# Optimization experiments

Hardware: AMD Instinct MI355X
Metric: run time of the kernel (lower is better)

## Reference

```python
import jax, jax.numpy as jnp
import numpy as np

B, L, E, H, RR, BIO, NT, V, R = 16, 128, 256, 256, 128, 64, 3, 30000, 25


def setup_inputs() -> dict:
    key = jax.random.key(0)
    ks = jax.random.split(key, 24)
    s = 0.05
    n = jax.random.normal
    inp = {
        'tokens': jax.random.randint(ks[0], (B, L), 0, V),
        'bio_gold': jax.random.randint(ks[1], (B, L), 0, NT),
        'selection_gold': jax.random.uniform(ks[2], (B, L, R, L), jnp.float32),
        'word_emb': n(ks[3], (V, E), jnp.float32) * s,
        'W_ih_f': n(ks[4], (4 * H, E), jnp.float32) * s,
        'W_hh_f': n(ks[5], (4 * H, H), jnp.float32) * s,
        'b_f': n(ks[6], (4 * H,), jnp.float32) * s,
        'W_ih_b': n(ks[7], (4 * H, E), jnp.float32) * s,
        'W_hh_b': n(ks[8], (4 * H, H), jnp.float32) * s,
        'b_b': n(ks[9], (4 * H,), jnp.float32) * s,
        'emi_W': n(ks[10], (NT, H), jnp.float32) * s,
        'emi_b': n(ks[11], (NT,), jnp.float32) * s,
        'bio_emb': n(ks[12], (NT + 1, BIO), jnp.float32) * s,
        'sel_u_W': n(ks[13], (RR, H + BIO), jnp.float32) * s,
        'sel_u_b': n(ks[14], (RR,), jnp.float32) * s,
        'sel_v_W': n(ks[15], (RR, H + BIO), jnp.float32) * s,
        'sel_v_b': n(ks[16], (RR,), jnp.float32) * s,
        'sel_uv_W': n(ks[17], (RR, 2 * RR), jnp.float32) * s,
        'sel_uv_b': n(ks[18], (RR,), jnp.float32) * s,
        'rel_emb': n(ks[19], (R, RR), jnp.float32) * s,
        'crf_start': n(ks[20], (NT,), jnp.float32) * s,
        'crf_end': n(ks[21], (NT,), jnp.float32) * s,
        'crf_trans': n(ks[22], (NT, NT), jnp.float32) * s,
    }
    return inp


def _lstm(x, W_ih, W_hh, b, reverse):
    # x: [B,L,E] -> hidden states [B,L,H]; PyTorch gate order i,f,g,o
    Bb = x.shape[0]
    Hh = W_hh.shape[1]
    xg = jnp.swapaxes(jnp.einsum('ble,ge->blg', x, W_ih) + b, 0, 1)  # [L,B,4H]

    def step(carry, xt):
        h, c = carry
        g = xt + h @ W_hh.T
        i, f, gg, o = jnp.split(g, 4, axis=-1)
        c = jax.nn.sigmoid(f) * c + jax.nn.sigmoid(i) * jnp.tanh(gg)
        h = jax.nn.sigmoid(o) * jnp.tanh(c)
        return (h, c), h

    init = (jnp.zeros((Bb, Hh), x.dtype), jnp.zeros((Bb, Hh), x.dtype))
    _, hs = jax.lax.scan(step, init, xg, reverse=reverse)
    return jnp.swapaxes(hs, 0, 1)


def reference(tokens, bio_gold, selection_gold, word_emb, W_ih_f, W_hh_f, b_f,
              W_ih_b, W_hh_b, b_b, emi_W, emi_b, bio_emb, sel_u_W, sel_u_b,
              sel_v_W, sel_v_b, sel_uv_W, sel_uv_b, rel_emb, crf_start,
              crf_end, crf_trans):
    mask = tokens != 0  # pad id 0
    maskf = mask.astype(jnp.float32)
    emb = word_emb[tokens]
    # BiLSTM, halves averaged as in (fwd + bwd) / 2
    o = (_lstm(emb, W_ih_f, W_hh_f, b_f, False)
         + _lstm(emb, W_ih_b, W_hh_b, b_b, True)) * 0.5
    emi = o @ emi_W.T + emi_b  # [B,L,NT]

    # ---- CRF negative log-likelihood (torchcrf, reduction='mean') ----
    bidx = jnp.arange(tokens.shape[0])
    e_sel = jnp.take_along_axis(emi, bio_gold[..., None], axis=2)[..., 0]  # [B,L]
    num = crf_start[bio_gold[:, 0]] + e_sel[:, 0]
    tr = crf_trans[bio_gold[:, :-1], bio_gold[:, 1:]]  # [B,L-1]
    num = num + ((tr + e_sel[:, 1:]) * maskf[:, 1:]).sum(1)
    seq_ends = jnp.maximum(mask.sum(1) - 1, 0)
    num = num + crf_end[bio_gold[bidx, seq_ends]]

    def crf_step(score, inp):
        emi_t, m_t = inp
        nxt = jax.nn.logsumexp(score[:, :, None] + crf_trans[None] + emi_t[:, None, :], axis=1)
        return jnp.where(m_t[:, None], nxt, score), None

    score0 = crf_start + emi[:, 0]
    score, _ = jax.lax.scan(crf_step, score0,
                            (jnp.swapaxes(emi[:, 1:], 0, 1), jnp.swapaxes(mask[:, 1:], 0, 1)))
    den = jax.nn.logsumexp(score + crf_end, axis=1)
    crf_loss = -(num - den).mean()

    # ---- pairwise biaffine selection head ----
    oc = jnp.concatenate([o, bio_emb[bio_gold]], axis=-1)  # [B,L,H+BIO]
    u = jax.nn.relu(oc @ sel_u_W.T + sel_u_b)  # [B,L,RR]
    v = jax.nn.relu(oc @ sel_v_W.T + sel_v_b)
    Rr = rel_emb.shape[1]
    W1, W2 = sel_uv_W[:, :Rr], sel_uv_W[:, Rr:]  # split cat([u,v]) linear
    a = u @ W1.T  # indexed by j (u was expanded along dim 1)
    c = v @ W2.T  # indexed by i
    uv = jax.nn.relu(a[:, None, :, :] + c[:, :, None, :] + sel_uv_b)  # [B,L,L,RR]
    logits = jnp.einsum('bijh,rh->birj', uv, rel_emb)  # [B,L,R,L]

    y = selection_gold
    bce = jnp.maximum(logits, 0) - logits * y + jnp.log1p(jnp.exp(-jnp.abs(logits)))
    selmask = maskf[:, :, None, None] * maskf[:, None, None, :]  # [B,L,1,L]
    sel_loss = (bce * selmask).sum() / maskf.sum()
    return crf_loss + sel_loss
```

## Files before the change

### kernel.cpp

```cpp
#include <hip/hip_runtime.h>
#include <cstdint>
#include <cstddef>


typedef __attribute__((ext_vector_type(8))) short short8;
typedef __attribute__((ext_vector_type(8))) int i32x8;
typedef __attribute__((ext_vector_type(4))) float f32x4;

__device__ __forceinline__ unsigned short f2bf(float f) {
  unsigned int u = __float_as_uint(f);
  u += 0x7fffu + ((u >> 16) & 1u);
  return (unsigned short)(u >> 16);
}
__device__ __forceinline__ float bf2f(unsigned short u) {
  return __uint_as_float(((unsigned int)u) << 16);
}

__device__ __forceinline__ void dev_pp8k128(const float* __restrict__ W,
                                            unsigned int* __restrict__ out, int idx) {
  int c = idx & 3;
  int lane = (idx >> 2) & 63;
  int f = idx >> 8;
  int nt = f >> 1, kt = f & 1;
  int n = nt * 16 + (lane & 15);
  int k0 = kt * 128 + (lane >> 4) * 32 + c * 8;
  const float* wp = &W[(size_t)n * 256 + k0];
  int lo = 0, hi = 0;
  lo = __builtin_amdgcn_cvt_pk_fp8_f32(wp[0], wp[1], lo, false);
  lo = __builtin_amdgcn_cvt_pk_fp8_f32(wp[2], wp[3], lo, true);
  hi = __builtin_amdgcn_cvt_pk_fp8_f32(wp[4], wp[5], hi, false);
  hi = __builtin_amdgcn_cvt_pk_fp8_f32(wp[6], wp[7], hi, true);
  size_t base = ((size_t)(f << 6) + lane) * 8 + (c << 1);
  out[base] = (unsigned)lo;
  out[base + 1] = (unsigned)hi;
}

__device__ __forceinline__ void dev_ppw(const float* __restrict__ W, int ldw, int nkt,
                                        uint4* __restrict__ out, int idx) {
  int lane = idx & 63;
  int f = idx >> 6;
  int kt = f % nkt;
  int nt = f / nkt;
  int row = nt * 16 + (lane & 15);
  int k0 = kt * 32 + ((lane >> 4) << 3);
  const float* wp = &W[(size_t)row * ldw + k0];
  union { unsigned short us[8]; uint4 v; } tmp;
#pragma unroll
  for (int j = 0; j < 8; ++j) tmp.us[j] = f2bf(wp[j]);
  out[idx] = tmp.v;
}

__global__ __launch_bounds__(256) void k_setup(
    const float* __restrict__ Whhf, unsigned int* __restrict__ wpk8f,
    const float* __restrict__ Whhb, unsigned int* __restrict__ wpk8b,
    const float* __restrict__ Wihf, uint4* __restrict__ wihfPk,
    const float* __restrict__ Wihb, uint4* __restrict__ wihbPk,
    const float* __restrict__ suW, uint4* __restrict__ suPk,
    const float* __restrict__ svW, uint4* __restrict__ svPk,
    const float* __restrict__ suvW, uint4* __restrict__ w1Pk, uint4* __restrict__ w2Pk,
    float* __restrict__ acc) {
  int bid = blockIdx.x;
  int t = threadIdx.x;
  if (bid < 128) {
    dev_pp8k128(Whhf, wpk8f, bid * 256 + t);
  } else if (bid < 256) {
    dev_pp8k128(Whhb, wpk8b, (bid - 128) * 256 + t);
  } else if (bid < 384) {
    dev_ppw(Wihf, 256, 8, wihfPk, (bid - 256) * 256 + t);
  } else if (bid < 512) {
    dev_ppw(Wihb, 256, 8, wihbPk, (bid - 384) * 256 + t);
  } else if (bid < 532) {
    dev_ppw(suW, 320, 10, suPk, (bid - 512) * 256 + t);
  } else if (bid < 552) {
    dev_ppw(svW, 320, 10, svPk, (bid - 532) * 256 + t);
  } else if (bid < 560) {
    dev_ppw(suvW, 256, 4, w1Pk, (bid - 552) * 256 + t);
  } else if (bid < 568) {
    dev_ppw(suvW + 128, 256, 4, w2Pk, (bid - 560) * 256 + t);
  } else {
    if (t < 16) acc[t] = 0.f;
  }
}

__global__ __launch_bounds__(256) void k_xg(
    const int* __restrict__ tok, const float* __restrict__ wemb,
    const uint4* __restrict__ WpkF, const float* __restrict__ biasF,
    unsigned short* __restrict__ CF,
    const uint4* __restrict__ WpkB, const float* __restrict__ biasB,
    unsigned short* __restrict__ CB) {
  const uint4* Wp = blockIdx.z ? WpkB : WpkF;
  const float* bi = blockIdx.z ? biasB : biasF;
  unsigned short* Co = blockIdx.z ? CB : CF;
  int bn = blockIdx.x, bm = blockIdx.y;
  int tid = threadIdx.x;
  int w = tid >> 6;
  int lane = tid & 63;
  int m = lane & 15;
  int q = lane >> 4;
  int arow = bm * 64 + w * 16 + m;
  const float* ew = wemb + (size_t)tok[arow] * 256 + (q << 3);
  f32x4 z = {0.f, 0.f, 0.f, 0.f};
  f32x4 ac[4] = {z, z, z, z};
  for (int kt = 0; kt < 8; ++kt) {
    float4 e0 = *reinterpret_cast<const float4*>(ew + (kt << 5));
    float4 e1 = *reinterpret_cast<const float4*>(ew + (kt << 5) + 4);
    union { unsigned short us[8]; short8 v; } af;
    af.us[0] = f2bf(e0.x); af.us[1] = f2bf(e0.y); af.us[2] = f2bf(e0.z); af.us[3] = f2bf(e0.w);
    af.us[4] = f2bf(e1.x); af.us[5] = f2bf(e1.y); af.us[6] = f2bf(e1.z); af.us[7] = f2bf(e1.w);
#pragma unroll
    for (int nt = 0; nt < 4; ++nt) {
      uint4 b4 = Wp[(size_t)(((bn << 2) + nt) * 8 + kt) * 64 + lane];
      ac[nt] = __builtin_amdgcn_mfma_f32_16x16x32_bf16(af.v, __builtin_bit_cast(short8, b4), ac[nt], 0, 0, 0);
    }
  }
#pragma unroll
  for (int nt = 0; nt < 4; ++nt) {
    int col = (bn << 6) + (nt << 4) + m;
    float bv = bi[col];
#pragma unroll
    for (int reg = 0; reg < 4; ++reg) {
      int row = (bm << 6) + (w << 4) + (q << 2) + reg;
      Co[(size_t)row * 1024 + col] = f2bf(ac[nt][reg] + bv);
    }
  }
}

__global__ __launch_bounds__(512, 2) void k_lstm8(
    const unsigned short* __restrict__ xgf, const unsigned short* __restrict__ xgb,
    const unsigned int* __restrict__ wpkf, const unsigned int* __restrict__ wpkb,
    unsigned short* __restrict__ hsf, unsigned short* __restrict__ hsb) {
  int bid = blockIdx.x;
  int dir = bid >> 4;
  int b = bid & 15;
  const unsigned short* xg = (dir ? xgb : xgf) + (size_t)b * 128 * 1024;
  const unsigned int* wpk = dir ? wpkb : wpkf;
  unsigned short* hseq = (dir ? hsb : hsf) + (size_t)b * 128 * 256;

  __shared__ __align__(16) unsigned short xgl[8 * 1024];
  __shared__ __align__(16) unsigned short hfl[8 * 256];
  __shared__ __align__(16) unsigned char h8[2][256];

  int tid = threadIdx.x;
  int w = tid >> 6;
  int lane = tid & 63;
  int m = lane & 15;
  int q = lane >> 4;

  i32x8 wfr[4][2][2];
#pragma unroll
  for (int g = 0; g < 4; ++g)
#pragma unroll
    for (int n = 0; n < 2; ++n)
#pragma unroll
      for (int kt = 0; kt < 2; ++kt) {
        int f = (((g << 4) + (w << 1) + n) << 1) + kt;
        wfr[g][n][kt] = *reinterpret_cast<const i32x8*>(wpk + (((size_t)(f << 6) + lane) << 3));
      }
#pragma unroll
  for (int g = 0; g < 4; ++g)
#pragma unroll
    for (int n = 0; n < 2; ++n)
#pragma unroll
      for (int kt = 0; kt < 2; ++kt)
        asm volatile("" : "+v"(wfr[g][n][kt]));

  if (tid < 128) reinterpret_cast<unsigned int*>(&h8[0][0])[tid] = 0u;
  {
    int tb0 = dir ? 120 : 0;
#pragma unroll
    for (int r2 = 0; r2 < 2; ++r2) {
      uint4 x0v = *reinterpret_cast<const uint4*>(
          (const char*)xg + (size_t)tb0 * 2048 + (size_t)(tid + (r2 << 9)) * 16);
      reinterpret_cast<uint4*>(xgl)[tid + (r2 << 9)] = x0v;
    }
  }
  __syncthreads();

  const f32x4 zero4 = {0.f, 0.f, 0.f, 0.f};
  float cst[2] = {0.f, 0.f};
  int j0 = (w << 5) + m;

  for (int c = 0; c < 16; ++c) {
    int tbase = dir ? (120 - 8 * c) : (8 * c);
    uint4 xnext0 = {0, 0, 0, 0}, xnext1 = {0, 0, 0, 0};
    if (c < 15) {
      int tb2 = dir ? (tbase - 8) : (tbase + 8);
      xnext0 = *reinterpret_cast<const uint4*>(
          (const char*)xg + (size_t)tb2 * 2048 + (size_t)tid * 16);
      xnext1 = *reinterpret_cast<const uint4*>(
          (const char*)xg + (size_t)tb2 * 2048 + (size_t)(tid + 512) * 16);
    }
#pragma unroll
    for (int i = 0; i < 8; ++i) {
      int s = 8 * c + i;
      int t = dir ? (127 - s) : s;
      int slot = t & 7;
      const unsigned char* cur = h8[s & 1];
      unsigned char* nxt = h8[(s & 1) ^ 1];

      i32x8 afr[2];
#pragma unroll
      for (int kt = 0; kt < 2; ++kt) {
        union { uint4 u[2]; i32x8 v; } tmp;
        const unsigned char* hp = cur + kt * 128 + q * 32;
        tmp.u[0] = *reinterpret_cast<const uint4*>(hp);
        tmp.u[1] = *reinterpret_cast<const uint4*>(hp + 16);
        afr[kt] = tmp.v;
      }

      float xv[4][2];
#pragma unroll
      for (int g = 0; g < 4; ++g)
#pragma unroll
        for (int n = 0; n < 2; ++n)
          xv[g][n] = bf2f(xgl[slot * 1024 + (g << 8) + j0 + (n << 4)]);

      f32x4 acg[4][2];
#pragma unroll
      for (int n = 0; n < 2; ++n) {
#pragma unroll
        for (int g = 0; g < 4; ++g)
          acg[g][n] = __builtin_amdgcn_mfma_scale_f32_16x16x128_f8f6f4(
              afr[0], wfr[g][n][0], zero4, 0, 0, 0, 0x7f7f7f7f, 0, 0x7f7f7f7f);
#pragma unroll
        for (int g = 0; g < 4; ++g)
          acg[g][n] = __builtin_amdgcn_mfma_scale_f32_16x16x128_f8f6f4(
              afr[1], wfr[g][n][1], acg[g][n], 0, 0, 0, 0x7f7f7f7f, 0, 0x7f7f7f7f);
      }

#pragma unroll
      for (int n = 0; n < 2; ++n) {
        float gi = acg[0][n][0] + xv[0][n];
        float gf = acg[1][n][0] + xv[1][n];
        float gg = acg[2][n][0] + xv[2][n];
        float go = acg[3][n][0] + xv[3][n];
        float si = __fdividef(1.f, 1.f + __expf(-gi));
        float sf = __fdividef(1.f, 1.f + __expf(-gf));
        float so = __fdividef(1.f, 1.f + __expf(-go));
        float tg = 1.f - __fdividef(2.f, __expf(2.f * gg) + 1.f);
        float cc = sf * cst[n] + si * tg;
        cst[n] = cc;
        float th = 1.f - __fdividef(2.f, __expf(2.f * cc) + 1.f);
        float h = so * th;
        if (q == 0) {
          hfl[slot * 256 + j0 + (n << 4)] = f2bf(h);
          int pk = __builtin_amdgcn_cvt_pk_fp8_f32(h, h, 0, false);
          nxt[j0 + (n << 4)] = (unsigned char)(pk & 0xff);
        }
      }
      asm volatile("s_waitcnt lgkmcnt(0)" ::: "memory");
      __builtin_amdgcn_s_barrier();
      asm volatile("" ::: "memory");
    }
    if (tid < 256) {
      int trow = tid >> 5;
      int jf = (tid & 31) << 3;
      uint4 hv = reinterpret_cast<const uint4*>(hfl)[tid];
      *reinterpret_cast<uint4*>(hseq + (size_t)(tbase + trow) * 256 + jf) = hv;
    }
    if (c < 15) {
      reinterpret_cast<uint4*>(xgl)[tid] = xnext0;
      reinterpret_cast<uint4*>(xgl)[tid + 512] = xnext1;
      __syncthreads();
    }
  }
}

__global__ __launch_bounds__(256) void k_mid2(
    const unsigned short* __restrict__ hf16, const unsigned short* __restrict__ hb16,
    const int* __restrict__ bio, const float* __restrict__ bioE,
    const float* __restrict__ emiW, const float* __restrict__ emib,
    const uint4* __restrict__ suPk, const float* __restrict__ sub,
    const uint4* __restrict__ svPk, const float* __restrict__ svb,
    const uint4* __restrict__ w1Pk, const uint4* __restrict__ w2Pk,
    unsigned short* __restrict__ a16, unsigned short* __restrict__ c16,
    float* __restrict__ emi) {
  __shared__ __align__(16) unsigned short oc[16][328];
  __shared__ __align__(16) unsigned short ub[16][136];
  __shared__ __align__(16) unsigned short vb[16][136];
  int r0 = blockIdx.x * 16;
  int tid = threadIdx.x;

#pragma unroll
  for (int it = 0; it < 8; ++it) {
    int i = it * 256 + tid;
    int row = i >> 7, h2 = (i & 127) << 1;
    unsigned int af = *reinterpret_cast<const unsigned int*>(hf16 + (size_t)(r0 + row) * 256 + h2);
    unsigned int ab = *reinterpret_cast<const unsigned int*>(hb16 + (size_t)(r0 + row) * 256 + h2);
    float lo = 0.5f * (bf2f((unsigned short)af) + bf2f((unsigned short)ab));
    float hi = 0.5f * (bf2f((unsigned short)(af >> 16)) + bf2f((unsigned short)(ab >> 16)));
    unsigned int pk = (unsigned int)f2bf(lo) | ((unsigned int)f2bf(hi) << 16);
    *reinterpret_cast<unsigned int*>(&oc[row][h2]) = pk;
  }
#pragma unroll
  for (int it = 0; it < 2; ++it) {
    int i = it * 256 + tid;
    int row = i >> 5, p = (i & 31) << 1;
    int bi = bio[r0 + row];
    float b0 = bioE[bi * 64 + p], b1 = bioE[bi * 64 + p + 1];
    unsigned int pk = (unsigned int)f2bf(b0) | ((unsigned int)f2bf(b1) << 16);
    *reinterpret_cast<unsigned int*>(&oc[row][256 + p]) = pk;
  }
  __syncthreads();

  if (tid < 192) {
    int did = tid >> 2, sub4 = tid & 3;
    int row = did / 3, g = did - row * 3;
    const float* ew = emiW + g * 256 + sub4 * 64;
    float av = 0.f;
#pragma unroll
    for (int k = 0; k < 64; ++k) av += bf2f(oc[row][sub4 * 64 + k]) * ew[k];
    av += __shfl_xor(av, 1);
    av += __shfl_xor(av, 2);
    if (sub4 == 0) emi[(size_t)(r0 + row) * 3 + g] = av + emib[g];
  }

  int w = tid >> 6, lane = tid & 63, m = lane & 15, q = lane >> 4;
  {
    f32x4 z = {0.f, 0.f, 0.f, 0.f};
    f32x4 au[2] = {z, z}, av2[2] = {z, z};
    for (int kt = 0; kt < 10; ++kt) {
      uint4 a4 = *reinterpret_cast<const uint4*>(&oc[m][(kt << 5) + (q << 3)]);
      short8 af = __builtin_bit_cast(short8, a4);
#pragma unroll
      for (int d = 0; d < 2; ++d) {
        int nt = (w << 1) + d;
        uint4 bu = suPk[(size_t)(nt * 10 + kt) * 64 + lane];
        uint4 bv = svPk[(size_t)(nt * 10 + kt) * 64 + lane];
        au[d] = __builtin_amdgcn_mfma_f32_16x16x32_bf16(af, __builtin_bit_cast(short8, bu), au[d], 0, 0, 0);
        av2[d] = __builtin_amdgcn_mfma_f32_16x16x32_bf16(af, __builtin_bit_cast(short8, bv), av2[d], 0, 0, 0);
      }
    }
#pragma unroll
    for (int d = 0; d < 2; ++d) {
      int col = ((w << 1) + d) * 16 + m;
      float bu = sub[col], bv = svb[col];
#pragma unroll
      for (int reg = 0; reg < 4; ++reg) {
        int row = (q << 2) + reg;
        ub[row][col] = f2bf(fmaxf(au[d][reg] + bu, 0.f));
        vb[row][col] = f2bf(fmaxf(av2[d][reg] + bv, 0.f));
      }
    }
  }
  __syncthreads();

  {
    f32x4 z = {0.f, 0.f, 0.f, 0.f};
    f32x4 aa[2] = {z, z}, cc[2] = {z, z};
    for (int kt = 0; kt < 4; ++kt) {
      uint4 ua = *reinterpret_cast<const uint4*>(&ub[m][(kt << 5) + (q << 3)]);
      uint4 va = *reinterpret_cast<const uint4*>(&vb[m][(kt << 5) + (q << 3)]);
      short8 uf = __builtin_bit_cast(short8, ua);
      short8 vf = __builtin_bit_cast(short8, va);
#pragma unroll
      for (int d = 0; d < 2; ++d) {
        int nt = (w << 1) + d;
        uint4 b1 = w1Pk[(size_t)((nt << 2) + kt) * 64 + lane];
        uint4 b2 = w2Pk[(size_t)((nt << 2) + kt) * 64 + lane];
        aa[d] = __builtin_amdgcn_mfma_f32_16x16x32_bf16(uf, __builtin_bit_cast(short8, b1), aa[d], 0, 0, 0);
        cc[d] = __builtin_amdgcn_mfma_f32_16x16x32_bf16(vf, __builtin_bit_cast(short8, b2), cc[d], 0, 0, 0);
      }
    }
#pragma unroll
    for (int d = 0; d < 2; ++d) {
      int col = ((w << 1) + d) * 16 + m;
#pragma unroll
      for (int reg = 0; reg < 4; ++reg) {
        int row = r0 + (q << 2) + reg;
        a16[(size_t)row * 128 + col] = f2bf(aa[d][reg]);
        c16[(size_t)row * 128 + col] = f2bf(cc[d][reg]);
      }
    }
  }
}

__global__ __launch_bounds__(256) void k_loss(
    const unsigned short* __restrict__ a16, const unsigned short* __restrict__ c16,
    const float* __restrict__ suvb, const float* __restrict__ rel,
    const float* __restrict__ y, const int* __restrict__ tok,
    const float* __restrict__ emi, const int* __restrict__ bio,
    const float* __restrict__ cstart, const float* __restrict__ cend,
    const float* __restrict__ ctrans,
    float* __restrict__ acc, float* __restrict__ out) {
  int blk = blockIdx.x;
  int tid = threadIdx.x;
  if (blk < 1024) {
    __shared__ unsigned short alds[128][136];
    __shared__ float cbs[2][128];
    __shared__ float red[4];
    int b = blk >> 6;
    int ip = blk & 63;
    int hh = tid & 127;
    int half = tid >> 7;
#pragma unroll
    for (int it = 0; it < 32; ++it) {
      int idx = it * 256 + tid;
      int jrow = idx >> 6;
      int h2 = (idx & 63) << 1;
      unsigned int av = *reinterpret_cast<const unsigned int*>(
          a16 + ((size_t)(b << 7) + jrow) * 128 + h2);
      alds[h2][jrow] = (unsigned short)av;
      alds[h2 + 1][jrow] = (unsigned short)(av >> 16);
    }
    {
      int i = (ip << 1) + half;
      cbs[half][hh] = bf2f(c16[(size_t)((b << 7) + i) * 128 + hh]) + suvb[hh];
    }
    __syncthreads();
    int i = (ip << 1) + half;
    int j = hh;
    float lg[25];
#pragma unroll
    for (int r = 0; r < 25; ++r) lg[r] = 0.f;
    for (int h = 0; h < 128; ++h) {
      float av = bf2f(alds[h][j]);
      float uv = fmaxf(av + cbs[half][h], 0.f);
#pragma unroll
      for (int r = 0; r < 25; ++r) lg[r] += uv * rel[r * 128 + h];
    }
    float mi = (tok[(b << 7) + i] != 0) ? 1.f : 0.f;
    float mj = (tok[(b << 7) + j] != 0) ? 1.f : 0.f;
    const float* yp = y + (size_t)((b << 7) + i) * 3200 + j;
    float bs = 0.f;
#pragma unroll
    for (int r = 0; r < 25; ++r) {
      float x = lg[r];
      float yv = yp[r * 128];
      bs += fmaxf(x, 0.f) - x * yv + __logf(1.f + __expf(-fabsf(x)));
    }
    bs *= mi * mj;
#pragma unroll
    for (int off = 32; off; off >>= 1) bs += __shfl_down(bs, off);
    if ((tid & 63) == 0) red[tid >> 6] = bs;
    __syncthreads();
    if (tid == 0) atomicAdd(&acc[0], red[0] + red[1] + red[2] + red[3]);
  } else {
    __shared__ float elds[128][4];
    __shared__ float msk[128];
    __shared__ int biol[128];
    __shared__ float r_t[2], r_m[2];
    int b = blk - 1024;
    int t = tid;
    if (t < 128) {
      biol[t] = bio[b * 128 + t];
      msk[t] = (tok[b * 128 + t] != 0) ? 1.f : 0.f;
#pragma unroll
      for (int g = 0; g < 3; ++g) elds[t][g] = emi[(b * 128 + t) * 3 + g];
    }
    __syncthreads();
    if (t < 128) {
      float m = msk[t];
      float term;
      if (t == 0)
        term = cstart[biol[0]] + elds[0][biol[0]];
      else
        term = (ctrans[biol[t - 1] * 3 + biol[t]] + elds[t][biol[t]]) * m;
      float ms = m;
#pragma unroll
      for (int off = 32; off; off >>= 1) {
        term += __shfl_down(term, off);
        ms += __shfl_down(ms, off);
      }
      if ((t & 63) == 0) { r_t[t >> 6] = term; r_m[t >> 6] = ms; }
    }
    __syncthreads();
    if (t == 0) {
      float num = r_t[0] + r_t[1];
      float msum = r_m[0] + r_m[1];
      int se = (int)msum - 1;
      if (se < 0) se = 0;
      num += cend[biol[se]];
      float tr[9];
#pragma unroll
      for (int i2 = 0; i2 < 9; ++i2) tr[i2] = ctrans[i2];
      float s0 = cstart[0] + elds[0][0];
      float s1 = cstart[1] + elds[0][1];
      float s2 = cstart[2] + elds[0][2];
      for (int tt = 1; tt < 128; ++tt) {
        float a0, a1, a2, mx, n0, n1, n2;
        a0 = s0 + tr[0]; a1 = s1 + tr[3]; a2 = s2 + tr[6];
        mx = fmaxf(a0, fmaxf(a1, a2));
        n0 = mx + __logf(__expf(a0 - mx) + __expf(a1 - mx) + __expf(a2 - mx)) + elds[tt][0];
        a0 = s0 + tr[1]; a1 = s1 + tr[4]; a2 = s2 + tr[7];
        mx = fmaxf(a0, fmaxf(a1, a2));
        n1 = mx + __logf(__expf(a0 - mx) + __expf(a1 - mx) + __expf(a2 - mx)) + elds[tt][1];
        a0 = s0 + tr[2]; a1 = s1 + tr[5]; a2 = s2 + tr[8];
        mx = fmaxf(a0, fmaxf(a1, a2));
        n2 = mx + __logf(__expf(a0 - mx) + __expf(a1 - mx) + __expf(a2 - mx)) + elds[tt][2];
        if (msk[tt] != 0.f) { s0 = n0; s1 = n1; s2 = n2; }
      }
      float a0 = s0 + cend[0], a1 = s1 + cend[1], a2 = s2 + cend[2];
      float mx = fmaxf(a0, fmaxf(a1, a2));
      float den = mx + __logf(__expf(a0 - mx) + __expf(a1 - mx) + __expf(a2 - mx));
      atomicAdd(&acc[1], num - den);
      atomicAdd(&acc[2], msum);
    }
  }
  if (tid == 0) {
    __threadfence();
    unsigned old = atomicAdd((unsigned int*)(acc + 5), 1u);
    if (old == 1039u) {
      __threadfence();
      float s0 = atomicAdd(&acc[0], 0.f);
      float s1 = atomicAdd(&acc[1], 0.f);
      float s2 = atomicAdd(&acc[2], 0.f);
      out[0] = -(s1 * (1.f / 16.f)) + s0 / s2;
    }
  }
}

extern "C" void kernel_launch(void* const* d_in, const int* in_sizes, int n_in,
                              void* d_out, int out_size, void* d_ws, size_t ws_size,
                              hipStream_t stream) {
  const int* tokens = (const int*)d_in[0];
  const int* bio = (const int*)d_in[1];
  const float* selg = (const float*)d_in[2];
  const float* wemb = (const float*)d_in[3];
  const float* Wihf = (const float*)d_in[4];
  const float* Whhf = (const float*)d_in[5];
  const float* bf = (const float*)d_in[6];
  const float* Wihb = (const float*)d_in[7];
  const float* Whhb = (const float*)d_in[8];
  const float* bb = (const float*)d_in[9];
  const float* emiW = (const float*)d_in[10];
  const float* emib = (const float*)d_in[11];
  const float* bioE = (const float*)d_in[12];
  const float* suW = (const float*)d_in[13];
  const float* sub = (const float*)d_in[14];
  const float* svW = (const float*)d_in[15];
  const float* svb = (const float*)d_in[16];
  const float* suvW = (const float*)d_in[17];
  const float* suvb = (const float*)d_in[18];
  const float* rel = (const float*)d_in[19];
  const float* cstart = (const float*)d_in[20];
  const float* cend = (const float*)d_in[21];
  const float* ctrans = (const float*)d_in[22];

  float* ws = (float*)d_ws;
  float* xgf16 = ws;
  float* xgb16 = xgf16 + 1048576;
  float* hf16 = xgb16 + 1048576;
  float* hb16 = hf16 + 262144;
  float* a16 = hb16 + 262144;
  float* c16 = a16 + 131072;
  float* emi = c16 + 131072;
  float* wpk8f = emi + 6144;
  float* wpk8b = wpk8f + 65536;
  float* wihfPk = wpk8b + 65536;
  float* wihbPk = wihfPk + 131072;
  float* suPk = wihbPk + 131072;
  float* svPk = suPk + 20480;
  float* w1Pk = svPk + 20480;
  float* w2Pk = w1Pk + 8192;
  float* acc = w2Pk + 8192;

  k_setup<<<569, 256, 0, stream>>>(
      Whhf, (unsigned int*)wpk8f, Whhb, (unsigned int*)wpk8b,
      Wihf, (uint4*)wihfPk, Wihb, (uint4*)wihbPk,
      suW, (uint4*)suPk, svW, (uint4*)svPk,
      suvW, (uint4*)w1Pk, (uint4*)w2Pk, acc);

  k_xg<<<dim3(16, 32, 2), 256, 0, stream>>>(
      tokens, wemb,
      (const uint4*)wihfPk, bf, (unsigned short*)xgf16,
      (const uint4*)wihbPk, bb, (unsigned short*)xgb16);

  k_lstm8<<<32, 512, 0, stream>>>(
      (const unsigned short*)xgf16, (const unsigned short*)xgb16,
      (const unsigned int*)wpk8f, (const unsigned int*)wpk8b,
      (unsigned short*)hf16, (unsigned short*)hb16);

  k_mid2<<<128, 256, 0, stream>>>(
      (const unsigned short*)hf16, (const unsigned short*)hb16,
      bio, bioE, emiW, emib,
      (const uint4*)suPk, sub, (const uint4*)svPk, svb,
      (const uint4*)w1Pk, (const uint4*)w2Pk,
      (unsigned short*)a16, (unsigned short*)c16, emi);

  k_loss<<<1040, 256, 0, stream>>>((const unsigned short*)a16, (const unsigned short*)c16,
                                   suvb, rel, selg, tokens, emi, bio,
                                   cstart, cend, ctrans, acc, (float*)d_out);
}
```

Before: 394.2 us.

## Repack LSTM input gates per lane and prefetch them from global directly

k_xg now writes the input-gate projections in a per-lane packed layout, so each LSTM lane fetches all eight of its gate values (4 gates x 2 columns) with a single 16-byte global load. The recurrent kernel drops its LDS staging of xg and of the h sequence, prefetches x one step ahead in registers, and writes h straight to global. It also raises wave priority around the MFMA block. This removes the per-chunk block syncs and LDS traffic from the serial recurrence, at the cost of global-load latency on each step and scattered 2-byte global stores.

```diff
diff --git a/kernel.cpp b/kernel.cpp
--- a/kernel.cpp
+++ b/kernel.cpp
@@ -85,12 +85,12 @@
 __global__ __launch_bounds__(256) void k_xg(
     const int* __restrict__ tok, const float* __restrict__ wemb,
     const uint4* __restrict__ WpkF, const float* __restrict__ biasF,
-    unsigned short* __restrict__ CF,
+    unsigned short* __restrict__ PF,
     const uint4* __restrict__ WpkB, const float* __restrict__ biasB,
-    unsigned short* __restrict__ CB) {
+    unsigned short* __restrict__ PB) {
   const uint4* Wp = blockIdx.z ? WpkB : WpkF;
   const float* bi = blockIdx.z ? biasB : biasF;
-  unsigned short* Co = blockIdx.z ? CB : CF;
+  unsigned short* Po = blockIdx.z ? PB : PF;
   int bn = blockIdx.x, bm = blockIdx.y;
   int tid = threadIdx.x;
   int w = tid >> 6;
@@ -117,34 +117,42 @@
   for (int nt = 0; nt < 4; ++nt) {
     int col = (bn << 6) + (nt << 4) + m;
     float bv = bi[col];
+    int g = col >> 8;
+    int cell = col & 255;
+    int wl = cell >> 5;
+    int nn = (cell >> 4) & 1;
+    int mm = cell & 15;
 #pragma unroll
     for (int reg = 0; reg < 4; ++reg) {
       int row = (bm << 6) + (w << 4) + (q << 2) + reg;
-      Co[(size_t)row * 1024 + col] = f2bf(ac[nt][reg] + bv);
-    }
-  }
-}
-
-__global__ __launch_bounds__(512, 2) void k_lstm8(
-    const unsigned short* __restrict__ xgf, const unsigned short* __restrict__ xgb,
+      int b = row >> 7;
+      int t = row & 127;
+      size_t pidx = ((size_t)b << 17) +
+                    (size_t)(((t << 7) + (wl << 4) + mm) << 3) + (g << 1) + nn;
+      Po[pidx] = f2bf(ac[nt][reg] + bv);
+    }
+  }
+}
+
+__global__ __launch_bounds__(512, 2) void k_lstm(
+    const unsigned short* __restrict__ Pf, const unsigned short* __restrict__ Pb,
     const unsigned int* __restrict__ wpkf, const unsigned int* __restrict__ wpkb,
     unsigned short* __restrict__ hsf, unsigned short* __restrict__ hsb) {
   int bid = blockIdx.x;
   int dir = bid >> 4;
   int b = bid & 15;
-  const unsigned short* xg = (dir ? xgb : xgf) + (size_t)b * 128 * 1024;
+  const unsigned short* P = (dir ? Pb : Pf) + ((size_t)b << 17);
   const unsigned int* wpk = dir ? wpkb : wpkf;
   unsigned short* hseq = (dir ? hsb : hsf) + (size_t)b * 128 * 256;
 
-  __shared__ __align__(16) unsigned short xgl[8 * 1024];
-  __shared__ __align__(16) unsigned short hfl[8 * 256];
-  __shared__ __align__(16) unsigned char h8[2][256];
+  __shared__ __align__(16) unsigned char h8[2][272];
 
   int tid = threadIdx.x;
   int w = tid >> 6;
   int lane = tid & 63;
   int m = lane & 15;
   int q = lane >> 4;
+  int j0 = (w << 5) + m;
 
   i32x8 wfr[4][2][2];
 #pragma unroll
@@ -164,76 +172,60 @@
       for (int kt = 0; kt < 2; ++kt)
         asm volatile("" : "+v"(wfr[g][n][kt]));
 
-  if (tid < 128) reinterpret_cast<unsigned int*>(&h8[0][0])[tid] = 0u;
-  {
-    int tb0 = dir ? 120 : 0;
-#pragma unroll
-    for (int r2 = 0; r2 < 2; ++r2) {
-      uint4 x0v = *reinterpret_cast<const uint4*>(
-          (const char*)xg + (size_t)tb0 * 2048 + (size_t)(tid + (r2 << 9)) * 16);
-      reinterpret_cast<uint4*>(xgl)[tid + (r2 << 9)] = x0v;
-    }
-  }
+  if (tid < 136) reinterpret_cast<unsigned int*>(&h8[0][0])[tid] = 0u;
   __syncthreads();
 
   const f32x4 zero4 = {0.f, 0.f, 0.f, 0.f};
   float cst[2] = {0.f, 0.f};
-  int j0 = (w << 5) + m;
-
-  for (int c = 0; c < 16; ++c) {
-    int tbase = dir ? (120 - 8 * c) : (8 * c);
-    uint4 xnext0 = {0, 0, 0, 0}, xnext1 = {0, 0, 0, 0};
-    if (c < 15) {
-      int tb2 = dir ? (tbase - 8) : (tbase + 8);
-      xnext0 = *reinterpret_cast<const uint4*>(
-          (const char*)xg + (size_t)tb2 * 2048 + (size_t)tid * 16);
-      xnext1 = *reinterpret_cast<const uint4*>(
-          (const char*)xg + (size_t)tb2 * 2048 + (size_t)(tid + 512) * 16);
-    }
-#pragma unroll
-    for (int i = 0; i < 8; ++i) {
-      int s = 8 * c + i;
-      int t = dir ? (127 - s) : s;
-      int slot = t & 7;
-      const unsigned char* cur = h8[s & 1];
-      unsigned char* nxt = h8[(s & 1) ^ 1];
-
-      i32x8 afr[2];
-#pragma unroll
-      for (int kt = 0; kt < 2; ++kt) {
-        union { uint4 u[2]; i32x8 v; } tmp;
-        const unsigned char* hp = cur + kt * 128 + q * 32;
-        tmp.u[0] = *reinterpret_cast<const uint4*>(hp);
-        tmp.u[1] = *reinterpret_cast<const uint4*>(hp + 16);
-        afr[kt] = tmp.v;
-      }
-
-      float xv[4][2];
+
+  auto load_x = [&](int s) -> uint4 {
+    int t = dir ? (127 - (s & 127)) : (s & 127);
+    return *reinterpret_cast<const uint4*>(
+        P + ((size_t)((t << 7) + (w << 4) + m) << 3));
+  };
+
+  auto step = [&](int s, uint4 x4) {
+    int t = dir ? (127 - s) : s;
+    const unsigned char* cur = &h8[s & 1][0];
+    unsigned char* nxt = &h8[(s & 1) ^ 1][0];
+
+    i32x8 afr[2];
+#pragma unroll
+    for (int kt = 0; kt < 2; ++kt) {
+      union { uint4 u[2]; i32x8 v; } tmp;
+      const unsigned char* hp = cur + kt * 128 + q * 32;
+      tmp.u[0] = *reinterpret_cast<const uint4*>(hp);
+      tmp.u[1] = *reinterpret_cast<const uint4*>(hp + 16);
+      afr[kt] = tmp.v;
+    }
+
+    f32x4 acg[4][2];
+    __builtin_amdgcn_s_setprio(1);
+#pragma unroll
+    for (int n = 0; n < 2; ++n) {
 #pragma unroll
       for (int g = 0; g < 4; ++g)
-#pragma unroll
-        for (int n = 0; n < 2; ++n)
-          xv[g][n] = bf2f(xgl[slot * 1024 + (g << 8) + j0 + (n << 4)]);
-
-      f32x4 acg[4][2];
+        acg[g][n] = __builtin_amdgcn_mfma_scale_f32_16x16x128_f8f6f4(
+            afr[0], wfr[g][n][0], zero4, 0, 0, 0, 0x7f7f7f7f, 0, 0x7f7f7f7f);
+#pragma unroll
+      for (int g = 0; g < 4; ++g)
+        acg[g][n] = __builtin_amdgcn_mfma_scale_f32_16x16x128_f8f6f4(
+            afr[1], wfr[g][n][1], acg[g][n], 0, 0, 0, 0x7f7f7f7f, 0, 0x7f7f7f7f);
+    }
+    __builtin_amdgcn_s_setprio(0);
+
+    if (q == 0) {
+      unsigned ug[4] = {x4.x, x4.y, x4.z, x4.w};
 #pragma unroll
       for (int n = 0; n < 2; ++n) {
-#pragma unroll
-        for (int g = 0; g < 4; ++g)
-          acg[g][n] = __builtin_amdgcn_mfma_scale_f32_16x16x128_f8f6f4(
-              afr[0], wfr[g][n][0], zero4, 0, 0, 0, 0x7f7f7f7f, 0, 0x7f7f7f7f);
-#pragma unroll
-        for (int g = 0; g < 4; ++g)
-          acg[g][n] = __builtin_amdgcn_mfma_scale_f32_16x16x128_f8f6f4(
-              afr[1], wfr[g][n][1], acg[g][n], 0, 0, 0, 0x7f7f7f7f, 0, 0x7f7f7f7f);
-      }
-
-#pragma unroll
-      for (int n = 0; n < 2; ++n) {
-        float gi = acg[0][n][0] + xv[0][n];
-        float gf = acg[1][n][0] + xv[1][n];
-        float gg = acg[2][n][0] + xv[2][n];
-        float go = acg[3][n][0] + xv[3][n];
+        float x0 = n ? __uint_as_float(ug[0] & 0xffff0000u) : __uint_as_float(ug[0] << 16);
+        float x1 = n ? __uint_as_float(ug[1] & 0xffff0000u) : __uint_as_float(ug[1] << 16);
+        float x2 = n ? __uint_as_float(ug[2] & 0xffff0000u) : __uint_as_float(ug[2] << 16);
+        float x3 = n ? __uint_as_float(ug[3] & 0xffff0000u) : __uint_as_float(ug[3] << 16);
+        float gi = acg[0][n][0] + x0;
+        float gf = acg[1][n][0] + x1;
+        float gg = acg[2][n][0] + x2;
+        float go = acg[3][n][0] + x3;
         float si = __fdividef(1.f, 1.f + __expf(-gi));
         float sf = __fdividef(1.f, 1.f + __expf(-gf));
         float so = __fdividef(1.f, 1.f + __expf(-go));
@@ -242,27 +234,23 @@
         cst[n] = cc;
         float th = 1.f - __fdividef(2.f, __expf(2.f * cc) + 1.f);
         float h = so * th;
-        if (q == 0) {
-          hfl[slot * 256 + j0 + (n << 4)] = f2bf(h);
-          int pk = __builtin_amdgcn_cvt_pk_fp8_f32(h, h, 0, false);
-          nxt[j0 + (n << 4)] = (unsigned char)(pk & 0xff);
-        }
-      }
-      asm volatile("s_waitcnt lgkmcnt(0)" ::: "memory");
-      __builtin_amdgcn_s_barrier();
-      asm volatile("" ::: "memory");
-    }
-    if (tid < 256) {
-      int trow = tid >> 5;
-      int jf = (tid & 31) << 3;
-      uint4 hv = reinterpret_cast<const uint4*>(hfl)[tid];
-      *reinterpret_cast<uint4*>(hseq + (size_t)(tbase + trow) * 256 + jf) = hv;
-    }
-    if (c < 15) {
-      reinterpret_cast<uint4*>(xgl)[tid] = xnext0;
-      reinterpret_cast<uint4*>(xgl)[tid + 512] = xnext1;
-      __syncthreads();
-    }
+        int j = j0 + (n << 4);
+        hseq[(size_t)t * 256 + j] = f2bf(h);
+        int pk = __builtin_amdgcn_cvt_pk_fp8_f32(h, h, 0, false);
+        nxt[j] = (unsigned char)(pk & 0xff);
+      }
+    }
+    asm volatile("s_waitcnt lgkmcnt(0)" ::: "memory");
+    __builtin_amdgcn_s_barrier();
+    asm volatile("" ::: "memory");
+  };
+
+  uint4 xA = load_x(0);
+  for (int sp = 0; sp < 128; sp += 2) {
+    uint4 xB = load_x(sp + 1);
+    step(sp, xA);
+    xA = load_x(sp + 2);
+    step(sp + 1, xB);
   }
 }
 
@@ -566,7 +554,7 @@
       (const uint4*)wihfPk, bf, (unsigned short*)xgf16,
       (const uint4*)wihbPk, bb, (unsigned short*)xgb16);
 
-  k_lstm8<<<32, 512, 0, stream>>>(
+  k_lstm<<<32, 512, 0, stream>>>(
       (const unsigned short*)xgf16, (const unsigned short*)xgb16,
       (const unsigned int*)wpk8f, (const unsigned int*)wpk8b,
       (unsigned short*)hf16, (unsigned short*)hb16);
```

After: 387.5 us. No clear change (-1.7%).
